# Optimization experiments

Measured on AMD Instinct MI355X. Metric: run time of the kernel, lower is better.

## Reference

```python
import jax, jax.numpy as jnp
import numpy as np

B, F, D = 1024, 64, 64  # batch, num fields, embedding dim


def setup_inputs() -> dict:
    key = jax.random.key(0)
    ks = jax.random.split(key, 7)
    return {
        "x": jax.random.normal(ks[0], (B, F, D), dtype=jnp.float32),
        "W1": jax.random.normal(ks[1], (F, F * F), dtype=jnp.float32) * 0.02,
        "b1": jax.random.normal(ks[2], (F,), dtype=jnp.float32) * 0.02,
        "W2": jax.random.normal(ks[3], (F, F * F), dtype=jnp.float32) * 0.02,
        "b2": jax.random.normal(ks[4], (F,), dtype=jnp.float32) * 0.02,
        "Wfc": jax.random.normal(ks[5], (1, 2 * F), dtype=jnp.float32) * 0.02,
        "bfc": jax.random.normal(ks[6], (1,), dtype=jnp.float32) * 0.02,
    }


def reference(x, W1, b1, W2, b2, Wfc, bfc):
    # x: [B, F, D]. CIN layer: outer product over field dims, 1x1 conv (channel
    # contraction with weight [F, F*F]), ReLU.
    b_, f0, d = x.shape
    x0 = x[:, :, None, :]  # [B, F, 1, D]
    h = x
    xs = []
    for W, b in ((W1, b1), (W2, b2)):
        z = (x0 * h[:, None, :, :]).reshape(b_, f0 * f0, d)  # [B, F*F, D]
        h = jax.nn.relu(jnp.einsum('oc,bcd->bod', W, z) + b[None, :, None])  # [B, F, D]
        xs.append(h)
    pooled = jnp.sum(jnp.concatenate(xs, axis=1), axis=2)  # [B, 2F] sum-pool over D
    return pooled @ Wfc.T + bfc  # [B, 1]
```

## Files before the change

### kernel.cpp

```cpp
#include <hip/hip_runtime.h>

typedef short s16x4 __attribute__((ext_vector_type(4)));
typedef short s16x8 __attribute__((ext_vector_type(8)));
typedef float f32x2 __attribute__((ext_vector_type(2)));
typedef float f32x16 __attribute__((ext_vector_type(16)));
typedef unsigned int u32x4 __attribute__((ext_vector_type(4)));

#define HT_STRIDE 72

__device__ __forceinline__ unsigned short f2bf(float f) {
    unsigned int u = __float_as_uint(f);
    u += 0x7fffu + ((u >> 16) & 1u);
    return (unsigned short)(u >> 16);
}
__device__ __forceinline__ float bf2f(unsigned short h) {
    return __uint_as_float(((unsigned int)h) << 16);
}
__device__ __forceinline__ unsigned int pk2bf_rne(float lo, float hi) {
    unsigned int a = __float_as_uint(lo);
    a += 0x7fffu + ((a >> 16) & 1u);
    unsigned int b = __float_as_uint(hi);
    b += 0x7fffu + ((b >> 16) & 1u);
    return (a >> 16) | (b & 0xffff0000u);
}

__global__ __launch_bounds__(256) void prepack_kernel(const float* __restrict__ W1,
                                                      const float* __restrict__ W2,
                                                      unsigned short* __restrict__ Wp) {
    __shared__ float sRow[4096];
    const int blk = blockIdx.x;
    const int l = blk >> 6, o = blk & 63;
    const float* W = l ? W2 : W1;
    const float4* src = (const float4*)(W + o * 4096);
    float4* dstL = (float4*)sRow;
#pragma unroll
    for (int r = 0; r < 4; ++r)
        dstL[r * 256 + threadIdx.x] = src[r * 256 + threadIdx.x];
    __syncthreads();
    const int oh = o & 3, oc = o >> 2;
#pragma unroll
    for (int s = 0; s < 2; ++s) {
        int sl = s * 256 + threadIdx.x;
        int lane = sl & 63;
        int ks = (sl >> 6) & 3;
        int jt = sl >> 8;
        int q2 = lane >> 5, n31 = lane & 31;
        const float* base = sRow + jt * 32 + n31;
        int i0 = 16 * ks + 8 * q2;
        u32x4 pv;
        pv[0] = pk2bf_rne(base[(i0 + 0) * 64], base[(i0 + 1) * 64]);
        pv[1] = pk2bf_rne(base[(i0 + 2) * 64], base[(i0 + 3) * 64]);
        pv[2] = pk2bf_rne(base[(i0 + 4) * 64], base[(i0 + 5) * 64]);
        pv[3] = pk2bf_rne(base[(i0 + 6) * 64], base[(i0 + 7) * 64]);
        int G = (((l * 4 + oh) * 16 + oc) * 2 + jt) * 4 + ks;
        ((u32x4*)Wp)[G * 64 + lane] = pv;
    }
}

__global__ __launch_bounds__(256, 2) void cin_kernel(const float* __restrict__ x,
                                                     const unsigned short* __restrict__ Wp,
                                                     const float* __restrict__ b1,
                                                     const float* __restrict__ b2,
                                                     const float* __restrict__ Wfc,
                                                     const float* __restrict__ bfc,
                                                     float* __restrict__ out) {
    __shared__ __align__(16) unsigned short sH[2][64 * HT_STRIDE];
    __shared__ float sBias[128], sWfc[128], sRed[4];

    const int tid = threadIdx.x;
    const int oh = tid >> 6;
    const int lane = tid & 63;
    const int q2 = lane >> 5;
    const int n31 = lane & 31;
    const int bb = blockIdx.x;

    {
        const float4* xb4 = (const float4*)(x + bb * 4096);
#pragma unroll
        for (int rr = 0; rr < 4; ++rr) {
            int e4 = rr * 256 + tid;
            float4 v = xb4[e4];
            int e = e4 << 2;
            int f = e >> 6;
            int d0 = e & 63;
            sH[0][(d0 + 0) * HT_STRIDE + f] = f2bf(v.x);
            sH[0][(d0 + 1) * HT_STRIDE + f] = f2bf(v.y);
            sH[0][(d0 + 2) * HT_STRIDE + f] = f2bf(v.z);
            sH[0][(d0 + 3) * HT_STRIDE + f] = f2bf(v.w);
        }
    }
    if (tid < 128) {
        sBias[tid] = (tid < 64) ? b1[tid] : b2[tid - 64];
        sWfc[tid] = Wfc[tid];
    }
    __syncthreads();

    const f32x16 zz = {};
    float contrib = 0.0f;
    const s16x8* WpS8 = (const s16x8*)Wp;

    s16x8 bfr[2][4];
#pragma unroll
    for (int nt = 0; nt < 2; ++nt) {
        const int d = nt * 32 + n31;
#pragma unroll
        for (int ks = 0; ks < 4; ++ks)
            bfr[nt][ks] = *(const s16x8*)&sH[0][d * HT_STRIDE + 16 * ks + 8 * q2];
    }

    for (int l = 0; l < 2; ++l) {
        if (l) __syncthreads();

        const unsigned short* hsrc = sH[l];
        f32x2 cw[2][2][8];
#pragma unroll
        for (int nt = 0; nt < 2; ++nt) {
            const int d = nt * 32 + n31;
#pragma unroll
            for (int jt = 0; jt < 2; ++jt)
#pragma unroll
                for (int m = 0; m < 4; ++m) {
                    s16x4 hv = *(const s16x4*)&hsrc[d * HT_STRIDE + jt * 32 + 4 * q2 + 8 * m];
                    cw[nt][jt][2 * m] = (f32x2){bf2f((unsigned short)hv[0]),
                                                bf2f((unsigned short)hv[1])};
                    cw[nt][jt][2 * m + 1] = (f32x2){bf2f((unsigned short)hv[2]),
                                                    bf2f((unsigned short)hv[3])};
                }
        }

        const s16x8* pW = WpS8 + (l * 4 + oh) * 128 * 64 + lane;
        s16x8 Areg[2][4];
#pragma unroll
        for (int ks = 0; ks < 4; ++ks) Areg[0][ks] = pW[ks * 64];
        f32x2 hp[2];

#pragma unroll 2
        for (int it = 0; it < 32; ++it) {
            const int jt = it & 1;
            const int o = 4 * (it >> 1) + oh;
            if (it < 31) {
                const s16x8* p = pW + (it + 1) * 4 * 64;
#pragma unroll
                for (int ks = 0; ks < 4; ++ks) Areg[(it + 1) & 1][ks] = p[ks * 64];
            }
            const s16x8* A = Areg[it & 1];

            f32x16 a0 = __builtin_amdgcn_mfma_f32_32x32x16_bf16(A[0], bfr[0][0], zz, 0, 0, 0);
            f32x16 a1 = __builtin_amdgcn_mfma_f32_32x32x16_bf16(A[0], bfr[1][0], zz, 0, 0, 0);
#pragma unroll
            for (int ks = 1; ks < 4; ++ks) {
                a0 = __builtin_amdgcn_mfma_f32_32x32x16_bf16(A[ks], bfr[0][ks], a0, 0, 0, 0);
                a1 = __builtin_amdgcn_mfma_f32_32x32x16_bf16(A[ks], bfr[1][ks], a1, 0, 0, 0);
            }

#pragma unroll
            for (int nt = 0; nt < 2; ++nt) {
                const f32x2* a2 = nt ? (const f32x2*)&a1 : (const f32x2*)&a0;
                f32x2 s = a2[0] * cw[nt][jt][0];
#pragma unroll
                for (int p = 1; p < 8; ++p) s += a2[p] * cw[nt][jt][p];
                if (jt == 0) {
                    hp[nt] = s;
                } else {
                    f32x2 t2 = hp[nt] + s;
                    float hsum = t2.x + t2.y;
                    hsum += __shfl_xor(hsum, 32, 64);
                    float v = fmaxf(hsum + sBias[l * 64 + o], 0.0f);
                    contrib += v * sWfc[l * 64 + o];
                    if (l == 0)
                        sH[1][(nt * 32 + n31) * HT_STRIDE + o] = f2bf(v);
                }
            }
        }
    }

    contrib *= 0.5f;
#pragma unroll
    for (int off = 32; off > 0; off >>= 1)
        contrib += __shfl_down(contrib, off, 64);
    if (lane == 0) sRed[oh] = contrib;
    __syncthreads();
    if (tid == 0)
        out[bb] = sRed[0] + sRed[1] + sRed[2] + sRed[3] + bfc[0];
}

extern "C" void kernel_launch(void* const* d_in, const int* in_sizes, int n_in,
                              void* d_out, int out_size, void* d_ws, size_t ws_size,
                              hipStream_t stream) {
    const float* x = (const float*)d_in[0];
    const float* W1 = (const float*)d_in[1];
    const float* b1 = (const float*)d_in[2];
    const float* W2 = (const float*)d_in[3];
    const float* b2 = (const float*)d_in[4];
    const float* Wfc = (const float*)d_in[5];
    const float* bfc = (const float*)d_in[6];
    float* out = (float*)d_out;

    unsigned short* Wp = (unsigned short*)d_ws;

    prepack_kernel<<<128, 256, 0, stream>>>(W1, W2, Wp);
    cin_kernel<<<1024, 256, 0, stream>>>(x, Wp, b1, b2, Wfc, bfc, out);
}
```

Measured before the change: 141.1 us.

## Process two batch rows per block and stage weights in LDS via async loads

Each block now handles two batch samples, so every packed weight tile is fetched once and reused across both samples, and the grid is halved. The weights are streamed chunk by chunk into a double-buffered LDS region with global_load_lds while the MFMAs consume the previous chunk. Waves are re-split by embedding-half and output-channel parity, and the layer-0 result overwrites the input tile in place. The cost is 64 block-wide barriers per block and about 50KB of LDS per block, which may limit occupancy and make the waves run in lockstep.

```diff
diff --git a/kernel.cpp b/kernel.cpp
--- a/kernel.cpp
+++ b/kernel.cpp
@@ -7,6 +7,7 @@
 typedef unsigned int u32x4 __attribute__((ext_vector_type(4)));
 
 #define HT_STRIDE 72
+#define CHUNK_ELEMS 8192
 
 __device__ __forceinline__ unsigned short f2bf(float f) {
     unsigned int u = __float_as_uint(f);
@@ -37,7 +38,6 @@
     for (int r = 0; r < 4; ++r)
         dstL[r * 256 + threadIdx.x] = src[r * 256 + threadIdx.x];
     __syncthreads();
-    const int oh = o & 3, oc = o >> 2;
 #pragma unroll
     for (int s = 0; s < 2; ++s) {
         int sl = s * 256 + threadIdx.x;
@@ -52,8 +52,21 @@
         pv[1] = pk2bf_rne(base[(i0 + 2) * 64], base[(i0 + 3) * 64]);
         pv[2] = pk2bf_rne(base[(i0 + 4) * 64], base[(i0 + 5) * 64]);
         pv[3] = pk2bf_rne(base[(i0 + 6) * 64], base[(i0 + 7) * 64]);
-        int G = (((l * 4 + oh) * 16 + oc) * 2 + jt) * 4 + ks;
+        int G = ((l * 64 + o) * 2 + jt) * 4 + ks;
         ((u32x4*)Wp)[G * 64 + lane] = pv;
+    }
+}
+
+__device__ __forceinline__ void stage_chunk(const unsigned short* g, unsigned short* s,
+                                            int w, int lane) {
+#pragma unroll
+    for (int r = 0; r < 4; ++r) {
+        const unsigned short* gp = g + w * 2048 + r * 512 + lane * 8;
+        unsigned short* lp = s + w * 2048 + r * 512;
+        __builtin_amdgcn_global_load_lds(
+            (const __attribute__((address_space(1))) unsigned int*)gp,
+            (__attribute__((address_space(3))) unsigned int*)lp,
+            16, 0, 0);
     }
 }
 
@@ -64,18 +77,23 @@
                                                      const float* __restrict__ Wfc,
                                                      const float* __restrict__ bfc,
                                                      float* __restrict__ out) {
+    __shared__ __align__(16) unsigned short sW[2 * CHUNK_ELEMS];
     __shared__ __align__(16) unsigned short sH[2][64 * HT_STRIDE];
-    __shared__ float sBias[128], sWfc[128], sRed[4];
+    __shared__ float sBias[128], sWfc[128], sRed[4][2];
 
     const int tid = threadIdx.x;
-    const int oh = tid >> 6;
+    const int w = tid >> 6;
     const int lane = tid & 63;
     const int q2 = lane >> 5;
     const int n31 = lane & 31;
+    const int nt = w & 1;
+    const int oh2 = w >> 1;
+    const int d = nt * 32 + n31;
     const int bb = blockIdx.x;
 
-    {
-        const float4* xb4 = (const float4*)(x + bb * 4096);
+#pragma unroll
+    for (int bl = 0; bl < 2; ++bl) {
+        const float4* xb4 = (const float4*)(x + (bb * 2 + bl) * 4096);
 #pragma unroll
         for (int rr = 0; rr < 4; ++rr) {
             int e4 = rr * 256 + tid;
@@ -83,105 +101,104 @@
             int e = e4 << 2;
             int f = e >> 6;
             int d0 = e & 63;
-            sH[0][(d0 + 0) * HT_STRIDE + f] = f2bf(v.x);
-            sH[0][(d0 + 1) * HT_STRIDE + f] = f2bf(v.y);
-            sH[0][(d0 + 2) * HT_STRIDE + f] = f2bf(v.z);
-            sH[0][(d0 + 3) * HT_STRIDE + f] = f2bf(v.w);
+            sH[bl][(d0 + 0) * HT_STRIDE + f] = f2bf(v.x);
+            sH[bl][(d0 + 1) * HT_STRIDE + f] = f2bf(v.y);
+            sH[bl][(d0 + 2) * HT_STRIDE + f] = f2bf(v.z);
+            sH[bl][(d0 + 3) * HT_STRIDE + f] = f2bf(v.w);
         }
     }
     if (tid < 128) {
         sBias[tid] = (tid < 64) ? b1[tid] : b2[tid - 64];
         sWfc[tid] = Wfc[tid];
     }
+    stage_chunk(Wp, sW, w, lane);
     __syncthreads();
 
     const f32x16 zz = {};
-    float contrib = 0.0f;
-    const s16x8* WpS8 = (const s16x8*)Wp;
+    float contrib0 = 0.0f, contrib1 = 0.0f;
 
     s16x8 bfr[2][4];
 #pragma unroll
-    for (int nt = 0; nt < 2; ++nt) {
-        const int d = nt * 32 + n31;
+    for (int b = 0; b < 2; ++b)
 #pragma unroll
         for (int ks = 0; ks < 4; ++ks)
-            bfr[nt][ks] = *(const s16x8*)&sH[0][d * HT_STRIDE + 16 * ks + 8 * q2];
-    }
-
-    for (int l = 0; l < 2; ++l) {
-        if (l) __syncthreads();
-
-        const unsigned short* hsrc = sH[l];
-        f32x2 cw[2][2][8];
-#pragma unroll
-        for (int nt = 0; nt < 2; ++nt) {
-            const int d = nt * 32 + n31;
+            bfr[b][ks] = *(const s16x8*)&sH[b][d * HT_STRIDE + 16 * ks + 8 * q2];
+
+    f32x2 cw[2][2][8];
+    auto load_cw = [&]() {
+#pragma unroll
+        for (int b = 0; b < 2; ++b)
 #pragma unroll
             for (int jt = 0; jt < 2; ++jt)
 #pragma unroll
                 for (int m = 0; m < 4; ++m) {
-                    s16x4 hv = *(const s16x4*)&hsrc[d * HT_STRIDE + jt * 32 + 4 * q2 + 8 * m];
-                    cw[nt][jt][2 * m] = (f32x2){bf2f((unsigned short)hv[0]),
-                                                bf2f((unsigned short)hv[1])};
-                    cw[nt][jt][2 * m + 1] = (f32x2){bf2f((unsigned short)hv[2]),
-                                                    bf2f((unsigned short)hv[3])};
+                    s16x4 hv = *(const s16x4*)&sH[b][d * HT_STRIDE + jt * 32 + 4 * q2 + 8 * m];
+                    cw[b][jt][2 * m] = (f32x2){bf2f((unsigned short)hv[0]),
+                                               bf2f((unsigned short)hv[1])};
+                    cw[b][jt][2 * m + 1] = (f32x2){bf2f((unsigned short)hv[2]),
+                                                   bf2f((unsigned short)hv[3])};
                 }
-        }
-
-        const s16x8* pW = WpS8 + (l * 4 + oh) * 128 * 64 + lane;
-        s16x8 Areg[2][4];
-#pragma unroll
-        for (int ks = 0; ks < 4; ++ks) Areg[0][ks] = pW[ks * 64];
+    };
+    load_cw();
+
+#pragma unroll 2
+    for (int c = 0; c < 64; ++c) {
+        __syncthreads();
+        if (c < 63) stage_chunk(Wp + (c + 1) * CHUNK_ELEMS,
+                                sW + ((c + 1) & 1) * CHUNK_ELEMS, w, lane);
+        if (c == 32) load_cw();
+
+        const int l = c >> 5;
+        const int o = ((c & 31) << 1) + oh2;
+        const unsigned short* sA = sW + (c & 1) * CHUNK_ELEMS + oh2 * 4096;
         f32x2 hp[2];
 
-#pragma unroll 2
-        for (int it = 0; it < 32; ++it) {
-            const int jt = it & 1;
-            const int o = 4 * (it >> 1) + oh;
-            if (it < 31) {
-                const s16x8* p = pW + (it + 1) * 4 * 64;
-#pragma unroll
-                for (int ks = 0; ks < 4; ++ks) Areg[(it + 1) & 1][ks] = p[ks * 64];
-            }
-            const s16x8* A = Areg[it & 1];
-
-            f32x16 a0 = __builtin_amdgcn_mfma_f32_32x32x16_bf16(A[0], bfr[0][0], zz, 0, 0, 0);
-            f32x16 a1 = __builtin_amdgcn_mfma_f32_32x32x16_bf16(A[0], bfr[1][0], zz, 0, 0, 0);
-#pragma unroll
-            for (int ks = 1; ks < 4; ++ks) {
-                a0 = __builtin_amdgcn_mfma_f32_32x32x16_bf16(A[ks], bfr[0][ks], a0, 0, 0, 0);
-                a1 = __builtin_amdgcn_mfma_f32_32x32x16_bf16(A[ks], bfr[1][ks], a1, 0, 0, 0);
-            }
-
-#pragma unroll
-            for (int nt = 0; nt < 2; ++nt) {
-                const f32x2* a2 = nt ? (const f32x2*)&a1 : (const f32x2*)&a0;
-                f32x2 s = a2[0] * cw[nt][jt][0];
-#pragma unroll
-                for (int p = 1; p < 8; ++p) s += a2[p] * cw[nt][jt][p];
+#pragma unroll
+        for (int jt = 0; jt < 2; ++jt) {
+            const s16x8* Ap = (const s16x8*)(sA + jt * 2048) + lane;
+            s16x8 A0 = Ap[0], A1 = Ap[64], A2 = Ap[128], A3 = Ap[192];
+            f32x16 a0 = __builtin_amdgcn_mfma_f32_32x32x16_bf16(A0, bfr[0][0], zz, 0, 0, 0);
+            f32x16 a1 = __builtin_amdgcn_mfma_f32_32x32x16_bf16(A0, bfr[1][0], zz, 0, 0, 0);
+            a0 = __builtin_amdgcn_mfma_f32_32x32x16_bf16(A1, bfr[0][1], a0, 0, 0, 0);
+            a1 = __builtin_amdgcn_mfma_f32_32x32x16_bf16(A1, bfr[1][1], a1, 0, 0, 0);
+            a0 = __builtin_amdgcn_mfma_f32_32x32x16_bf16(A2, bfr[0][2], a0, 0, 0, 0);
+            a1 = __builtin_amdgcn_mfma_f32_32x32x16_bf16(A2, bfr[1][2], a1, 0, 0, 0);
+            a0 = __builtin_amdgcn_mfma_f32_32x32x16_bf16(A3, bfr[0][3], a0, 0, 0, 0);
+            a1 = __builtin_amdgcn_mfma_f32_32x32x16_bf16(A3, bfr[1][3], a1, 0, 0, 0);
+
+#pragma unroll
+            for (int b = 0; b < 2; ++b) {
+                const f32x2* a2 = b ? (const f32x2*)&a1 : (const f32x2*)&a0;
+                f32x2 s = a2[0] * cw[b][jt][0];
+#pragma unroll
+                for (int p = 1; p < 8; ++p) s += a2[p] * cw[b][jt][p];
                 if (jt == 0) {
-                    hp[nt] = s;
+                    hp[b] = s;
                 } else {
-                    f32x2 t2 = hp[nt] + s;
+                    f32x2 t2 = hp[b] + s;
                     float hsum = t2.x + t2.y;
                     hsum += __shfl_xor(hsum, 32, 64);
                     float v = fmaxf(hsum + sBias[l * 64 + o], 0.0f);
-                    contrib += v * sWfc[l * 64 + o];
+                    if (b) contrib1 += v * sWfc[l * 64 + o];
+                    else   contrib0 += v * sWfc[l * 64 + o];
                     if (l == 0)
-                        sH[1][(nt * 32 + n31) * HT_STRIDE + o] = f2bf(v);
+                        sH[b][d * HT_STRIDE + o] = f2bf(v);
                 }
             }
         }
     }
 
-    contrib *= 0.5f;
-#pragma unroll
-    for (int off = 32; off > 0; off >>= 1)
-        contrib += __shfl_down(contrib, off, 64);
-    if (lane == 0) sRed[oh] = contrib;
+    contrib0 *= 0.5f;
+    contrib1 *= 0.5f;
+#pragma unroll
+    for (int off = 32; off > 0; off >>= 1) {
+        contrib0 += __shfl_down(contrib0, off, 64);
+        contrib1 += __shfl_down(contrib1, off, 64);
+    }
+    if (lane == 0) { sRed[w][0] = contrib0; sRed[w][1] = contrib1; }
     __syncthreads();
-    if (tid == 0)
-        out[bb] = sRed[0] + sRed[1] + sRed[2] + sRed[3] + bfc[0];
+    if (tid < 2)
+        out[bb * 2 + tid] = sRed[0][tid] + sRed[1][tid] + sRed[2][tid] + sRed[3][tid] + bfc[0];
 }
 
 extern "C" void kernel_launch(void* const* d_in, const int* in_sizes, int n_in,
@@ -199,5 +216,5 @@
     unsigned short* Wp = (unsigned short*)d_ws;
 
     prepack_kernel<<<128, 256, 0, stream>>>(W1, W2, Wp);
-    cin_kernel<<<1024, 256, 0, stream>>>(x, Wp, b1, b2, Wfc, bfc, out);
-}
+    cin_kernel<<<512, 256, 0, stream>>>(x, Wp, b1, b2, Wfc, bfc, out);
+}
```

Result: slower. 146.3 us (+3.7%).
